# Kernel optimization log

Hardware: AMD Instinct MI355X
Metric: run time of the kernel (lower is better)

## Reference

```python
import jax, jax.numpy as jnp
import numpy as np
from jax import lax

HUMAN_SIZE = 54
NUM_ACTIONS = 1
INPUT_SIZE = HUMAN_SIZE + NUM_ACTIONS  # 55, one_hot=True
RNN_SIZE = 1024
SOURCE_SEQ_LEN = 50
TARGET_SEQ_LEN = 25
BATCH = 1024


def setup_inputs() -> dict:
    key = jax.random.key(0)
    ks = jax.random.split(key, 8)
    s = 1.0 / np.sqrt(RNN_SIZE)
    return {
        "encoder_inputs": jax.random.normal(ks[0], (BATCH, SOURCE_SEQ_LEN, INPUT_SIZE), jnp.float32),
        "decoder_inputs": jax.random.normal(ks[1], (BATCH, TARGET_SEQ_LEN, INPUT_SIZE), jnp.float32),
        "W_ih": jax.random.uniform(ks[2], (3 * RNN_SIZE, INPUT_SIZE), jnp.float32, -s, s),
        "W_hh": jax.random.uniform(ks[3], (3 * RNN_SIZE, RNN_SIZE), jnp.float32, -s, s),
        "b_ih": jax.random.uniform(ks[4], (3 * RNN_SIZE,), jnp.float32, -s, s),
        "b_hh": jax.random.uniform(ks[5], (3 * RNN_SIZE,), jnp.float32, -s, s),
        "fc_w": jax.random.uniform(ks[6], (INPUT_SIZE, RNN_SIZE), jnp.float32, -s, s),
        "fc_b": jax.random.uniform(ks[7], (INPUT_SIZE,), jnp.float32, -s, s),
    }


def _gru_step(h, x, W_ih, W_hh, b_ih, b_hh):
    # torch.nn.GRUCell math
    gi = x @ W_ih.T + b_ih            # [B, 3H]
    gh = h @ W_hh.T + b_hh            # [B, 3H]
    i_r, i_z, i_n = jnp.split(gi, 3, axis=-1)
    h_r, h_z, h_n = jnp.split(gh, 3, axis=-1)
    r = jax.nn.sigmoid(i_r + h_r)
    z = jax.nn.sigmoid(i_z + h_z)
    n = jnp.tanh(i_n + r * h_n)
    return (1.0 - z) * n + z * h


def reference(encoder_inputs, decoder_inputs, W_ih, W_hh, b_ih, b_hh, fc_w, fc_b):
    B = encoder_inputs.shape[0]
    H = W_hh.shape[1]
    state0 = jnp.zeros((B, H), dtype=encoder_inputs.dtype)

    # Encoder: first source_seq_len-1 frames, time-major scan (dropout p=0 -> identity)
    enc_tm = jnp.swapaxes(encoder_inputs[:, : SOURCE_SEQ_LEN - 1], 0, 1)  # [S-1, B, In]

    def enc_step(h, x):
        return _gru_step(h, x, W_ih, W_hh, b_ih, b_hh), None

    state, _ = lax.scan(enc_step, state0, enc_tm)

    def dec_step(carry, _):
        h, inp = carry
        inp = lax.stop_gradient(inp)  # inp.detach()
        h = _gru_step(h, inp, W_ih, W_hh, b_ih, b_hh)
        out = inp + h @ fc_w.T + fc_b  # residual add
        return (h, out), out

    (_, _), outs = lax.scan(dec_step, (state, decoder_inputs[:, 0]), None, length=TARGET_SEQ_LEN)
    return jnp.swapaxes(outs, 0, 1)  # [B, T, In]
```

## Files before the change

### kernel.cpp

```cpp
#include <hip/hip_runtime.h>


typedef unsigned short ushort_t;
typedef __bf16 bf16x8 __attribute__((ext_vector_type(8)));
typedef float f32x4 __attribute__((ext_vector_type(4)));
typedef unsigned int u32x4 __attribute__((ext_vector_type(4)));

#define MFMA(a, b, c) __builtin_amdgcn_mfma_f32_16x16x32_bf16(a, b, c, 0, 0, 0)

static __device__ __forceinline__ ushort_t f2bf(float f) {
  union { float f; unsigned u; } x; x.f = f;
  unsigned r = x.u + 0x7fffu + ((x.u >> 16) & 1u);
  return (ushort_t)(r >> 16);
}
static __device__ __forceinline__ float sigmf(float x) { return 1.f / (1.f + __expf(-x)); }
static __device__ __forceinline__ float tanhf_(float x) { return 1.f - 2.f / (__expf(2.f * x) + 1.f); }

static __device__ __forceinline__ __amdgpu_buffer_rsrc_t mkrsrc(const void* p) {
  return __builtin_amdgcn_make_buffer_rsrc(const_cast<void*>(p), (short)0, -1, 0x00020000);
}
#if __has_builtin(__builtin_amdgcn_raw_buffer_load_b128)
static __device__ __forceinline__ bf16x8 ldb(__amdgpu_buffer_rsrc_t r, int voff) {
  u32x4 v = __builtin_amdgcn_raw_buffer_load_b128(r, voff, 0, 1);
  union { u32x4 u; bf16x8 b; } x; x.u = v; return x.b;
}
static __device__ __forceinline__ bf16x8 ldbc(__amdgpu_buffer_rsrc_t r, int voff) {
  u32x4 v = __builtin_amdgcn_raw_buffer_load_b128(r, voff, 0, 0);
  union { u32x4 u; bf16x8 b; } x; x.u = v; return x.b;
}
#else
static __device__ __forceinline__ bf16x8 ldb(__amdgpu_buffer_rsrc_t r, int voff) {
  union { unsigned u[4]; bf16x8 b; } x;
  x.u[0] = __builtin_amdgcn_raw_buffer_load_b32(r, voff, 0, 1);
  x.u[1] = __builtin_amdgcn_raw_buffer_load_b32(r, voff + 4, 0, 1);
  x.u[2] = __builtin_amdgcn_raw_buffer_load_b32(r, voff + 8, 0, 1);
  x.u[3] = __builtin_amdgcn_raw_buffer_load_b32(r, voff + 12, 0, 1);
  return x.b;
}
static __device__ __forceinline__ bf16x8 ldbc(__amdgpu_buffer_rsrc_t r, int voff) {
  union { unsigned u[4]; bf16x8 b; } x;
  x.u[0] = __builtin_amdgcn_raw_buffer_load_b32(r, voff, 0, 0);
  x.u[1] = __builtin_amdgcn_raw_buffer_load_b32(r, voff + 4, 0, 0);
  x.u[2] = __builtin_amdgcn_raw_buffer_load_b32(r, voff + 8, 0, 0);
  x.u[3] = __builtin_amdgcn_raw_buffer_load_b32(r, voff + 12, 0, 0);
  return x.b;
}
#endif

__global__ __launch_bounds__(512, 2)
void seq2seq_xcd(const float* __restrict__ enc, const float* __restrict__ dec,
                 const float* __restrict__ Wih, const float* __restrict__ Whh,
                 const float* __restrict__ b_ih, const float* __restrict__ b_hh,
                 const float* __restrict__ fcw, const float* __restrict__ fcb,
                 float* __restrict__ outp,
                 ushort_t* __restrict__ xg, ushort_t* __restrict__ hA,
                 ushort_t* __restrict__ innA, ushort_t* __restrict__ nG,
                 ushort_t* __restrict__ fcG, unsigned* cnt) {
  __shared__ ushort_t WrzL[65536];
  __shared__ ushort_t WiL[6144];
  __shared__ float scratchF[4096];
  __shared__ unsigned sgs;

  const int tid = threadIdx.x;
  const int w = tid >> 6, l = tid & 63;
  const int fr = l & 15, fq4 = l >> 4;

  if (tid == 0) {
    unsigned x;
    asm volatile("s_getreg_b32 %0, hwreg(HW_REG_XCC_ID, 0, 8)" : "=s"(x));
    x &= 7u;
    unsigned s = atomicAdd(&cnt[x * 64], 1u);
    sgs = (x << 8) | s;
  }
  __syncthreads();
  const int g = sgs >> 8, slot = sgs & 255;
  const bool isFC = (slot >= 24);

  unsigned* arr4 = cnt + (8 + g * 4 + (slot & 3)) * 64;
  unsigned* arrb = cnt + (8 + g * 4) * 64;
  auto fcpp = [&](int td) { return cnt + (48 + g * 25 + td) * 64; };

  ushort_t* hbase = hA + (size_t)g * 262144;
  auto hb = [&](int i) { return hbase + (size_t)i * 131072; };
  ushort_t* xgg = xg + (size_t)g * 49 * 8192;
  auto inng = [&](int i) { return innA + (size_t)(g * 2 + i) * 8192; };
  ushort_t* nGp = nG + (size_t)(g * 32 + slot) * 32768;
  ushort_t* fcGg = fcG + (size_t)g * 65536;

  for (int i = tid; i < 65536; i += 512) {
    int j = i & 7, ln = (i >> 3) & 63, jf = (i >> 9) & 1, gt = (i >> 10) & 1, kt = i >> 11;
    int col = gt * 1024 + slot * 32 + jf * 16 + (ln & 15);
    int k = kt * 32 + (ln >> 4) * 8 + j;
    WrzL[i] = f2bf(Whh[(size_t)col * 1024 + k]);
  }
  for (int i = tid; i < 6144; i += 512) {
    int j = i & 7, ln = (i >> 3) & 63, jf = (i >> 9) & 1, rem = i >> 10;
    int gt = rem % 3, kt = rem / 3;
    int col = gt * 1024 + slot * 32 + jf * 16 + (ln & 15);
    int k = kt * 32 + (ln >> 4) * 8 + j;
    WiL[i] = (k < 55) ? f2bf(Wih[(size_t)col * 55 + k]) : (ushort_t)0;
  }
  for (int i = tid; i < 32768; i += 512) {
    int j = i & 7, ln = (i >> 3) & 63, jf = (i >> 9) & 1, kt = i >> 10;
    int col = 2048 + slot * 32 + jf * 16 + (ln & 15);
    int k = kt * 32 + (ln >> 4) * 8 + j;
    nGp[i] = f2bf(Whh[(size_t)col * 1024 + k]);
  }
#pragma unroll
  for (int rep = 0; rep < 2; ++rep) {
    int t = slot + rep * 32;
    if (t < 49) {
      ushort_t* xp = xgg + (size_t)t * 8192;
      for (int i = tid; i < 8192; i += 512) {
        int sub = i & 7, row = (i >> 3) & 127, kc = i >> 10;
        int c = kc * 8 + sub;
        xp[i] = (c < 55) ? f2bf(enc[((size_t)(g * 128 + row) * 50 + t) * 55 + c]) : (ushort_t)0;
      }
    }
  }
  if (slot < 4) {
    ushort_t* ip = inng(0);
    for (int i = slot * 2048 + tid; i < (slot + 1) * 2048; i += 512) {
      int sub = i & 7, row = (i >> 3) & 127, kc = i >> 10;
      int c = kc * 8 + sub;
      ip[i] = (c < 55) ? f2bf(dec[(size_t)(g * 128 + row) * 1375 + c]) : (ushort_t)0;
    }
  }
  if (isFC) {
    for (int i = (slot - 24) * 8192 + tid; i < (slot - 23) * 8192; i += 512) {
      int j = i & 7, ln = (i >> 3) & 63, jf = (i >> 9) & 3, kt = i >> 11;
      int c = jf * 16 + (ln & 15);
      int k = kt * 32 + (ln >> 4) * 8 + j;
      fcGg[i] = (c < 55) ? f2bf(fcw[(size_t)c * 1024 + k]) : (ushort_t)0;
    }
  }

  float brz[2], bzz[2], bin[2], bhn[2];
#pragma unroll
  for (int jf = 0; jf < 2; ++jf) {
    int col = slot * 32 + jf * 16 + fr;
    brz[jf] = b_ih[col] + b_hh[col];
    bzz[jf] = b_ih[1024 + col] + b_hh[1024 + col];
    bin[jf] = b_ih[2048 + col];
    bhn[jf] = b_hh[2048 + col];
  }
  const int Rm = (slot >> 2) * 16;
  const int cn = slot & 3;
  const int colO = cn * 16 + fr;
  float fcbO = 0.f, inpO[4] = {0.f, 0.f, 0.f, 0.f};
  if (w == 0) {
    fcbO = (colO < 55) ? fcb[colO] : 0.f;
#pragma unroll
    for (int v = 0; v < 4; ++v)
      inpO[v] = (colO < 55) ? dec[(size_t)(g * 128 + Rm + fq4 * 4 + v) * 1375 + colO] : 0.f;
  }
  f32x4 hreg0 = (f32x4){0.f, 0.f, 0.f, 0.f};
  f32x4 hreg1 = (f32x4){0.f, 0.f, 0.f, 0.f};

  auto arrive = [&]() {
    __syncthreads();
    if (tid == 0) atomicAdd(arr4, 1u);
  };
  auto wait_rel = [&](unsigned k) {
    if (tid == 0) {
      for (;;) {
        unsigned s0 = __hip_atomic_load(arrb, __ATOMIC_RELAXED, __HIP_MEMORY_SCOPE_AGENT);
        unsigned s1 = __hip_atomic_load(arrb + 64, __ATOMIC_RELAXED, __HIP_MEMORY_SCOPE_AGENT);
        unsigned s2 = __hip_atomic_load(arrb + 128, __ATOMIC_RELAXED, __HIP_MEMORY_SCOPE_AGENT);
        unsigned s3 = __hip_atomic_load(arrb + 192, __ATOMIC_RELAXED, __HIP_MEMORY_SCOPE_AGENT);
        if (s0 + s1 + s2 + s3 >= 32u * k) break;
        __builtin_amdgcn_s_sleep(1);
      }
    }
    __syncthreads();
  };
  auto fc_wait = [&](int td) {
    if (tid == 0) {
      while (__hip_atomic_load(fcpp(td), __ATOMIC_RELAXED, __HIP_MEMORY_SCOPE_AGENT) < 32u)
        __builtin_amdgcn_s_sleep(1);
    }
    __syncthreads();
  };

  f32x4 av[12], nx0, nx1;
  bf16x8 pA0[4], pA1[4];
  bf16x8 pN0[4], pN1[4];
  bf16x8 pb0, pb1, pb2, pb3;

  __amdgpu_buffer_rsrc_t rnG = mkrsrc(nGp);

  auto xpart = [&](const ushort_t* xp) {
    __amdgpu_buffer_rsrc_t rx = mkrsrc(xp);
    const int R = (w & 3) * 32 + (w >> 2) * 16;
#pragma unroll
    for (int kt = 0; kt < 2; ++kt) {
      bf16x8 a = ldb(rx, ((kt * 4 + fq4) * 128 + R + fr) * 16);
      const ushort_t* bl = WiL + kt * 3072 + l * 8;
      bf16x8 br_0 = *(const bf16x8*)(bl);
      bf16x8 br_1 = *(const bf16x8*)(bl + 512);
      bf16x8 bz_0 = *(const bf16x8*)(bl + 1024);
      bf16x8 bz_1 = *(const bf16x8*)(bl + 1536);
      bf16x8 bn_0 = *(const bf16x8*)(bl + 2048);
      bf16x8 bn_1 = *(const bf16x8*)(bl + 2560);
      if (w < 4) {
        av[0] = MFMA(a, br_0, av[0]);
        av[1] = MFMA(a, br_1, av[1]);
        av[4] = MFMA(a, bz_0, av[4]);
        av[5] = MFMA(a, bz_1, av[5]);
      } else {
        av[2] = MFMA(a, br_0, av[2]);
        av[3] = MFMA(a, br_1, av[3]);
        av[6] = MFMA(a, bz_0, av[6]);
        av[7] = MFMA(a, bz_1, av[7]);
      }
      nx0 = MFMA(a, bn_0, nx0);
      nx1 = MFMA(a, bn_1, nx1);
    }
  };

  auto hpre = [&]() {
    const int kh = w >> 2;
#pragma unroll
    for (int i = 0; i < 4; ++i) {
      int kt = kh * 16 + i;
      pN0[i] = ldbc(rnG, kt * 2048 + l * 16);
      pN1[i] = ldbc(rnG, kt * 2048 + 1024 + l * 16);
    }
    const ushort_t* bl0 = WrzL + (kh * 16) * 2048 + l * 8;
    pb0 = *(const bf16x8*)(bl0);
    pb1 = *(const bf16x8*)(bl0 + 512);
    pb2 = *(const bf16x8*)(bl0 + 1024);
    pb3 = *(const bf16x8*)(bl0 + 1536);
  };

  auto hmain = [&](const ushort_t* hbp) {
    __amdgpu_buffer_rsrc_t r = mkrsrc(hbp);
    const int kh = w >> 2, R = (w & 3) * 32;
#pragma unroll
    for (int i = 0; i < 4; ++i) {
      int kt = kh * 16 + i;
      pA0[i] = ldb(r, ((kt * 4 + fq4) * 128 + R + fr) * 16);
      pA1[i] = ldb(r, ((kt * 4 + fq4) * 128 + R + 16 + fr) * 16);
    }
    bf16x8 br0 = pb0, br1 = pb1, bz0 = pb2, bz1 = pb3;
#pragma unroll
    for (int i = 0; i < 16; ++i) {
      int kt = kh * 16 + i;
      bf16x8 a0 = pA0[i & 3], a1 = pA1[i & 3];
      bf16x8 n0 = pN0[i & 3], n1 = pN1[i & 3];
      bf16x8 cr0 = br0, cr1 = br1, cz0 = bz0, cz1 = bz1;
      if (i < 15) {
        const ushort_t* bln = WrzL + (kt + 1) * 2048 + l * 8;
        br0 = *(const bf16x8*)(bln);
        br1 = *(const bf16x8*)(bln + 512);
        bz0 = *(const bf16x8*)(bln + 1024);
        bz1 = *(const bf16x8*)(bln + 1536);
      }
      if (i < 12) {
        int kp = kt + 4;
        pA0[i & 3] = ldb(r, ((kp * 4 + fq4) * 128 + R + fr) * 16);
        pA1[i & 3] = ldb(r, ((kp * 4 + fq4) * 128 + R + 16 + fr) * 16);
        pN0[i & 3] = ldbc(rnG, kp * 2048 + l * 16);
        pN1[i & 3] = ldbc(rnG, kp * 2048 + 1024 + l * 16);
      }
      av[0] = MFMA(a0, cr0, av[0]);
      av[2] = MFMA(a1, cr0, av[2]);
      av[1] = MFMA(a0, cr1, av[1]);
      av[3] = MFMA(a1, cr1, av[3]);
      av[4] = MFMA(a0, cz0, av[4]);
      av[6] = MFMA(a1, cz0, av[6]);
      av[5] = MFMA(a0, cz1, av[5]);
      av[7] = MFMA(a1, cz1, av[7]);
      av[8] = MFMA(a0, n0, av[8]);
      av[10] = MFMA(a1, n0, av[10]);
      av[9] = MFMA(a0, n1, av[9]);
      av[11] = MFMA(a1, n1, av[11]);
    }
  };

#define KXCH(LO0, LO1, HI0, HI1, TS)                                \
  do {                                                              \
    if (w >= 4) {                                                   \
      float* sp_ = scratchF + ((w - 4) * 64 + l) * 4;               \
      *(f32x4*)(sp_) = av[LO0];                                     \
      *(f32x4*)(sp_ + 1024) = av[LO1];                              \
    } else {                                                        \
      float* sp_ = scratchF + (w * 64 + l) * 4;                     \
      *(f32x4*)(sp_ + 2048) = av[HI0];                              \
      *(f32x4*)(sp_ + 3072) = av[HI1];                              \
    }                                                               \
    __syncthreads();                                                \
    if (w < 4) {                                                    \
      const float* sp_ = scratchF + (w * 64 + l) * 4;               \
      av[LO0] += *(const f32x4*)(sp_);                              \
      av[LO1] += *(const f32x4*)(sp_ + 1024);                       \
    } else {                                                        \
      const float* sp_ = scratchF + ((w - 4) * 64 + l) * 4;         \
      av[HI0] += *(const f32x4*)(sp_ + 2048);                       \
      av[HI1] += *(const f32x4*)(sp_ + 3072);                       \
    }                                                               \
    if (TS) __syncthreads();                                        \
  } while (0)

#define EPI(RV, ZV, NHV, NXV, JF, HC)                                  \
  do {                                                                 \
    const int kq_ = slot * 4 + (JF)*2 + (fr >> 3);                     \
    _Pragma("unroll") for (int v = 0; v < 4; ++v) {                    \
      float rr = sigmf(RV[v] + brz[JF]);                               \
      float zz = sigmf(ZV[v] + bzz[JF]);                               \
      float nn = tanhf_(NXV[v] + bin[JF] + rr * (NHV[v] + bhn[JF]));   \
      float h = (1.f - zz) * nn + zz * HC[v];                          \
      HC[v] = h;                                                       \
      int row_ = Rbase + fq4 * 4 + v;                                  \
      hn[(kq_ * 128 + row_) * 8 + sub_] = f2bf(h);                     \
    }                                                                  \
  } while (0)

  auto fcdo32 = [&](const ushort_t* hbp, int td, bool wr, ushort_t* innW) {
    __amdgpu_buffer_rsrc_t r = mkrsrc(hbp);
    __amdgpu_buffer_rsrc_t rf = mkrsrc(fcGg);
    bf16x8 Af[4], Bf[4];
#pragma unroll
    for (int i = 0; i < 4; ++i) {
      int kt = w * 4 + i;
      Af[i] = ldb(r, ((kt * 4 + fq4) * 128 + Rm + fr) * 16);
      Bf[i] = ldbc(rf, (kt * 4 + cn) * 1024 + l * 16);
    }
    f32x4 fa = (f32x4){0.f, 0.f, 0.f, 0.f};
#pragma unroll
    for (int i = 0; i < 4; ++i) fa = MFMA(Af[i], Bf[i], fa);
    *(f32x4*)(scratchF + (w * 64 + l) * 4) = fa;
    __syncthreads();
    if (w == 0) {
      f32x4 s = *(const f32x4*)(scratchF + l * 4);
#pragma unroll
      for (int ww = 1; ww < 8; ++ww)
        s += *(const f32x4*)(scratchF + (ww * 64 + l) * 4);
      const int kq = colO >> 3, sub = colO & 7;
#pragma unroll
      for (int v = 0; v < 4; ++v) {
        int row = Rm + fq4 * 4 + v;
        float o = s[v] + inpO[v] + fcbO;
        inpO[v] = o;
        if (wr) innW[(kq * 128 + row) * 8 + sub] = f2bf(o);
        if (colO < 55) outp[(size_t)(g * 128 + row) * 1375 + td * 55 + colO] = o;
      }
    }
    __syncthreads();
  };

  arrive();
  wait_rel(1);

  for (int t = 0; t < 74; ++t) {
#pragma unroll
    for (int i = 0; i < 12; ++i) av[i] = (f32x4){0.f, 0.f, 0.f, 0.f};
    nx0 = (f32x4){0.f, 0.f, 0.f, 0.f};
    nx1 = (f32x4){0.f, 0.f, 0.f, 0.f};

    if (t <= 49) {
      xpart(t <= 48 ? xgg + (size_t)t * 8192 : inng(0));
    }
    if (t > 0) {
      hpre();
      wait_rel(t + 1);
    }
    if (t >= 50) {
      fcdo32(hb(t & 1), t - 50, true, inng((t - 49) & 1));
      if (tid == 0) atomicAdd(fcpp(t - 50), 1u);
    }
    if (t > 0) hmain(hb(t & 1));
    if (t >= 50) {
      fc_wait(t - 50);
      xpart(inng((t - 49) & 1));
    }
    KXCH(0, 1, 2, 3, 1);
    KXCH(4, 5, 6, 7, 1);
    KXCH(8, 9, 10, 11, 0);
    {
      ushort_t* hn = hb((t + 1) & 1);
      const int Rbase = (w & 3) * 32 + (w >> 2) * 16;
      const int sub_ = fr & 7;
      if (w < 4) {
        EPI(av[0], av[4], av[8], nx0, 0, hreg0);
        EPI(av[1], av[5], av[9], nx1, 1, hreg1);
      } else {
        EPI(av[2], av[6], av[10], nx0, 0, hreg0);
        EPI(av[3], av[7], av[11], nx1, 1, hreg1);
      }
    }
    arrive();
  }

  wait_rel(75);
  fcdo32(hb(0), 24, false, (ushort_t*)0);
}

extern "C" void kernel_launch(void* const* d_in, const int* in_sizes, int n_in,
                              void* d_out, int out_size, void* d_ws, size_t ws_size,
                              hipStream_t stream) {
  const float* enc  = (const float*)d_in[0];
  const float* dec  = (const float*)d_in[1];
  const float* Wih  = (const float*)d_in[2];
  const float* Whh  = (const float*)d_in[3];
  const float* b_ih = (const float*)d_in[4];
  const float* b_hh = (const float*)d_in[5];
  const float* fcw  = (const float*)d_in[6];
  const float* fcb  = (const float*)d_in[7];
  float* out = (float*)d_out;

  char* ws = (char*)d_ws;
  unsigned* cnt  = (unsigned*)ws; ws += 65536;
  ushort_t* xg   = (ushort_t*)ws; ws += (size_t)8 * 49 * 8192 * 2;
  ushort_t* hA   = (ushort_t*)ws; ws += (size_t)8 * 2 * 131072 * 2;
  ushort_t* innA = (ushort_t*)ws; ws += (size_t)8 * 2 * 8192 * 2;
  ushort_t* nG   = (ushort_t*)ws; ws += (size_t)8 * 32 * 32768 * 2;
  ushort_t* fcG  = (ushort_t*)ws; ws += (size_t)8 * 65536 * 2;

  (void)hipMemsetAsync(cnt, 0, 65536, stream);
  seq2seq_xcd<<<256, 512, 0, stream>>>(
      enc, dec, Wih, Whh, b_ih, b_hh, fcw, fcb, out,
      xg, hA, innA, nG, fcG, cnt);
}
```

Measured before the change: 754.2 us.

## Hoist fc weights to registers, split h load, interleave exchange with epilogue

Loads the fc weight fragments once before the time loop into registers instead of reloading them every decoder step. Splits the hidden-state matmul into a load phase issued right after the barrier wait and a compute phase, so the h loads overlap the fc computation. Reorders the cross-wave accumulator exchanges so half the epilogue can run before the last exchange. This adds register pressure and relies on the exchange macro's sync semantics staying valid with the new ordering.

Result: slower. 790.3 us (+4.8%).

```diff
diff --git a/kernel.cpp b/kernel.cpp
--- a/kernel.cpp
+++ b/kernel.cpp
@@ -186,8 +186,10 @@
   bf16x8 pA0[4], pA1[4];
   bf16x8 pN0[4], pN1[4];
   bf16x8 pb0, pb1, pb2, pb3;
+  bf16x8 pF[4];
 
   __amdgpu_buffer_rsrc_t rnG = mkrsrc(nGp);
+  __amdgpu_buffer_rsrc_t rfG = mkrsrc(fcGg);
 
   auto xpart = [&](const ushort_t* xp) {
     __amdgpu_buffer_rsrc_t rx = mkrsrc(xp);
@@ -233,7 +235,7 @@
     pb3 = *(const bf16x8*)(bl0 + 1536);
   };
 
-  auto hmain = [&](const ushort_t* hbp) {
+  auto hload = [&](const ushort_t* hbp) {
     __amdgpu_buffer_rsrc_t r = mkrsrc(hbp);
     const int kh = w >> 2, R = (w & 3) * 32;
 #pragma unroll
@@ -242,6 +244,11 @@
       pA0[i] = ldb(r, ((kt * 4 + fq4) * 128 + R + fr) * 16);
       pA1[i] = ldb(r, ((kt * 4 + fq4) * 128 + R + 16 + fr) * 16);
     }
+  };
+
+  auto hrest = [&](const ushort_t* hbp) {
+    __amdgpu_buffer_rsrc_t r = mkrsrc(hbp);
+    const int kh = w >> 2, R = (w & 3) * 32;
     bf16x8 br0 = pb0, br1 = pb1, bz0 = pb2, bz1 = pb3;
 #pragma unroll
     for (int i = 0; i < 16; ++i) {
@@ -318,17 +325,15 @@
 
   auto fcdo32 = [&](const ushort_t* hbp, int td, bool wr, ushort_t* innW) {
     __amdgpu_buffer_rsrc_t r = mkrsrc(hbp);
-    __amdgpu_buffer_rsrc_t rf = mkrsrc(fcGg);
-    bf16x8 Af[4], Bf[4];
+    bf16x8 Af[4];
 #pragma unroll
     for (int i = 0; i < 4; ++i) {
       int kt = w * 4 + i;
       Af[i] = ldb(r, ((kt * 4 + fq4) * 128 + Rm + fr) * 16);
-      Bf[i] = ldbc(rf, (kt * 4 + cn) * 1024 + l * 16);
     }
     f32x4 fa = (f32x4){0.f, 0.f, 0.f, 0.f};
 #pragma unroll
-    for (int i = 0; i < 4; ++i) fa = MFMA(Af[i], Bf[i], fa);
+    for (int i = 0; i < 4; ++i) fa = MFMA(Af[i], pF[i], fa);
     *(f32x4*)(scratchF + (w * 64 + l) * 4) = fa;
     __syncthreads();
     if (w == 0) {
@@ -352,6 +357,12 @@
   arrive();
   wait_rel(1);
 
+  {
+#pragma unroll
+    for (int i = 0; i < 4; ++i)
+      pF[i] = ldbc(rfG, ((w * 4 + i) * 4 + cn) * 1024 + l * 16);
+  }
+
   for (int t = 0; t < 74; ++t) {
 #pragma unroll
     for (int i = 0; i < 12; ++i) av[i] = (f32x4){0.f, 0.f, 0.f, 0.f};
@@ -364,30 +375,28 @@
     if (t > 0) {
       hpre();
       wait_rel(t + 1);
+      hload(hb(t & 1));
     }
     if (t >= 50) {
       fcdo32(hb(t & 1), t - 50, true, inng((t - 49) & 1));
       if (tid == 0) atomicAdd(fcpp(t - 50), 1u);
     }
-    if (t > 0) hmain(hb(t & 1));
+    if (t > 0) hrest(hb(t & 1));
     if (t >= 50) {
       fc_wait(t - 50);
       xpart(inng((t - 49) & 1));
     }
-    KXCH(0, 1, 2, 3, 1);
-    KXCH(4, 5, 6, 7, 1);
-    KXCH(8, 9, 10, 11, 0);
+    KXCH(0, 4, 2, 6, 1);
+    KXCH(8, 1, 10, 3, 1);
     {
       ushort_t* hn = hb((t + 1) & 1);
       const int Rbase = (w & 3) * 32 + (w >> 2) * 16;
       const int sub_ = fr & 7;
-      if (w < 4) {
-        EPI(av[0], av[4], av[8], nx0, 0, hreg0);
-        EPI(av[1], av[5], av[9], nx1, 1, hreg1);
-      } else {
-        EPI(av[2], av[6], av[10], nx0, 0, hreg0);
-        EPI(av[3], av[7], av[11], nx1, 1, hreg1);
-      }
+      if (w < 4) EPI(av[0], av[4], av[8], nx0, 0, hreg0);
+      else       EPI(av[2], av[6], av[10], nx0, 0, hreg0);
+      KXCH(5, 9, 7, 11, 0);
+      if (w < 4) EPI(av[1], av[5], av[9], nx1, 1, hreg1);
+      else       EPI(av[3], av[7], av[11], nx1, 1, hreg1);
     }
     arrive();
   }
```
